# Kernel optimization log

Measured on AMD Instinct MI355X. Metric: run time of the kernel, lower is better.

## Reference

```python
import jax, jax.numpy as jnp
import numpy as np

B, N, E = 8, 2048, 2048  # requires N == E (see bmm(value, attn^T) constraint)

def setup_inputs() -> dict:
    key = jax.random.key(0)
    k1, k2, k3 = jax.random.split(key, 3)
    inputs = jax.random.normal(k1, (B, N, E), dtype=jnp.float32)
    # nn.Linear(embed_size, embed_size): weight [E,E], bias [E]
    W = jax.random.normal(k2, (E, E), dtype=jnp.float32) * (1.0 / np.sqrt(E))
    b = jax.random.normal(k3, (E,), dtype=jnp.float32) * 0.01
    gamma = jnp.zeros((), dtype=jnp.float32)  # nn.Parameter(torch.tensor(0.0))
    return {"inputs": inputs, "W": W, "b": b, "gamma": gamma}

def reference(inputs, W, b, gamma):
    # query = Linear(inputs); key = value = inputs
    query = jnp.einsum('bne,fe->bnf', inputs, W) + b          # [B,N,E]
    # scores = bmm(query, key^T) + gamma  -> [B,N,N]
    scores = jnp.einsum('bne,bme->bnm', query, inputs) + gamma
    # softmax over dim=1 (rows, NOT the usual last dim)
    attn = jax.nn.softmax(scores, axis=1)                      # [B,N,N]
    # output = bmm(value, attn^T): out[b,n,m] = sum_e value[b,n,e]*attn[b,m,e]
    out = jnp.einsum('bne,bme->bnm', inputs, attn)             # [B,N,N]
    return out
```

## Files before the change

kernel.cpp:

```cpp
#include <hip/hip_runtime.h>
#include <stdint.h>


typedef _Float16 f16;
typedef f16 f16x8 __attribute__((ext_vector_type(8)));
typedef f16 f16x4 __attribute__((ext_vector_type(4)));
typedef float f32x4 __attribute__((ext_vector_type(4)));

#define ND 2048
#define NNL 4194304L
#define NT 32

static __device__ __forceinline__ void stage16(const void* g, void* l) {
  __builtin_amdgcn_global_load_lds(
      (const __attribute__((address_space(1))) uint32_t*)g,
      (__attribute__((address_space(3))) uint32_t*)l, 16, 0, 0);
}

__global__ void cvt_f16(const float* __restrict__ x, f16* __restrict__ h, int n4) {
  int i = blockIdx.x * 256 + threadIdx.x;
  if (i >= n4) return;
  float4 v = reinterpret_cast<const float4*>(x)[i];
  f16x4 o;
  o.x = (f16)v.x; o.y = (f16)v.y; o.z = (f16)v.z; o.w = (f16)v.w;
  reinterpret_cast<f16x4*>(h)[i] = o;
}

#define RB(d_, o_, kh_) ((((d_) << 2) | ((o_) << 1) | (kh_)) * 16384)

#define STG(gp_, ro_, t_, kh_)                                           \
  do {                                                                   \
    stage16((gp_) + (long)(t_) * 128 + (kh_) * 64, smem + (ro_) + ld0);  \
    stage16((gp_) + 524288L + (long)(t_) * 128 + (kh_) * 64,             \
            smem + (ro_) + ld1);                                         \
  } while (0)

#define FENCE asm volatile("" ::: "memory")

#define SYNC(vm_)                                                        \
  do {                                                                   \
    asm volatile("s_waitcnt vmcnt(" #vm_ ") lgkmcnt(0)" ::: "memory");   \
    __builtin_amdgcn_s_barrier();                                        \
    FENCE;                                                               \
  } while (0)

#define PHASE(d_, mh_, kh_, RDB_, STAGE_)                                     \
  do {                                                                        \
    const char* ra_ = smem + RB(d_, 0, kh_) + (mh_) * 4096 + aoff;            \
    f16x8 af[4];                                                              \
    af[0] = *(const f16x8*)(ra_);                                             \
    af[1] = *(const f16x8*)(ra_ + 1024);                                      \
    af[2] = *(const f16x8*)(ra_ + 2048);                                      \
    af[3] = *(const f16x8*)(ra_ + 3072);                                      \
    if (RDB_) {                                                               \
      const char* rb_ = smem + RB(d_, 1, kh_) + boff;                         \
      bf[0] = *(const f16x8*)(rb_);                                           \
      bf[1] = *(const f16x8*)(rb_ + 1024);                                    \
      bf[2] = *(const f16x8*)(rb_ + 2048);                                    \
      bf[3] = *(const f16x8*)(rb_ + 3072);                                    \
    }                                                                         \
    STAGE_                                                                    \
    __builtin_amdgcn_s_setprio(1);                                            \
    _Pragma("unroll") for (int mt_ = 0; mt_ < 4; ++mt_) {                     \
      _Pragma("unroll") for (int nt_ = 0; nt_ < 4; ++nt_) {                   \
        acc[(mh_) * 4 + mt_][nt_] = __builtin_amdgcn_mfma_f32_16x16x32_f16(   \
            af[mt_], bf[nt_], acc[(mh_) * 4 + mt_][nt_], 0, 0, 0);            \
      }                                                                       \
    }                                                                         \
    __builtin_amdgcn_s_setprio(0);                                            \
  } while (0)

template <int MODE>
__launch_bounds__(512, 2) __global__
void gemm256(const f16* __restrict__ A, long sA, const f16* __restrict__ B, long sB,
             const float* __restrict__ bias, const float* __restrict__ gamma,
             float* __restrict__ Cf, f16* __restrict__ Ch,
             float* __restrict__ Mp, float* __restrict__ Sp) {
  __shared__ char smem[131072];

  const int bz = blockIdx.z;
  const int bx = ((blockIdx.x & 1) << 2) | (blockIdx.y & 3);
  const int by = (((blockIdx.x >> 1) & 3) << 1) | (blockIdx.y >> 2);
  const long tm = (long)by * 256;
  const long tn = (long)bx * 256;
  const int tid = threadIdx.x;
  const int lane = tid & 63;
  const int wid = tid >> 6;
  const int wm = (wid >> 2) << 7;
  const int wn = (wid & 3) << 6;

  const int sg = (tid & 3) ^ ((tid >> 3) & 3);
  const char* gA = (const char*)(A + bz * sA + tm * ND) + (long)(tid >> 2) * 4096 + sg * 16;
  const char* gB = (const char*)(B + bz * sB + tn * ND) + (long)(tid >> 2) * 4096 + sg * 16;
  const uint32_t ld0 = tid * 16u;
  const uint32_t ld1 = 8192u + tid * 16u;

  const int segsw = (((lane >> 4) ^ ((lane >> 1) & 3)) << 4);
  const int lrow = lane & 15;
  const int aoff = (wm + lrow) * 64 + segsw;
  const int boff = (wn + lrow) * 64 + segsw;

  f32x4 acc[8][4] = {};
  f16x8 bf[4];

  STG(gA, RB(0, 0, 0), 0, 0);
  STG(gB, RB(0, 1, 0), 0, 0);
  STG(gA, RB(0, 0, 1), 0, 1);
  STG(gB, RB(0, 1, 1), 0, 1);
  STG(gA, RB(1, 0, 0), 1, 0);
  STG(gB, RB(1, 1, 0), 1, 0);
  asm volatile("s_waitcnt vmcnt(8)" ::: "memory");
  __builtin_amdgcn_s_barrier();
  FENCE;

#pragma unroll 2
  for (int t = 0; t < NT - 2; ++t) {
    const int d = t & 1;
    const int e = d ^ 1;
    PHASE(d, 0, 0, 1, STG(gA, RB(e, 0, 1), t + 1, 1););
    PHASE(d, 1, 0, 0, STG(gB, RB(e, 1, 1), t + 1, 1););
    SYNC(8);
    PHASE(d, 0, 1, 1, STG(gA, RB(d, 0, 0), t + 2, 0););
    PHASE(d, 1, 1, 0, STG(gB, RB(d, 1, 0), t + 2, 0););
    SYNC(8);
  }
  {
    PHASE(0, 0, 0, 1, STG(gA, RB(1, 0, 1), NT - 1, 1););
    PHASE(0, 1, 0, 0, STG(gB, RB(1, 1, 1), NT - 1, 1););
    SYNC(8);
    PHASE(0, 0, 1, 1, ;);
    PHASE(0, 1, 1, 0, ;);
    SYNC(4);
  }
  {
    PHASE(1, 0, 0, 1, ;);
    PHASE(1, 1, 0, 0, ;);
    SYNC(0);
    PHASE(1, 0, 1, 1, ;);
    PHASE(1, 1, 1, 0, ;);
  }

  const int rr = (lane >> 4) << 2;
  const int cc = lane & 15;
  const long cb = (long)bz * NNL;
  if constexpr (MODE == 1) {
#pragma unroll
    for (int nt = 0; nt < 4; ++nt) {
      const long col = tn + wn + nt * 16 + cc;
      const float bj = bias[col];
#pragma unroll
      for (int mt = 0; mt < 8; ++mt) {
#pragma unroll
        for (int r = 0; r < 4; ++r) {
          const long row = tm + wm + mt * 16 + rr + r;
          Ch[cb + row * ND + col] = (f16)(acc[mt][nt][r] + bj);
        }
      }
    }
  } else if constexpr (MODE == 0) {
#pragma unroll
    for (int mt = 0; mt < 8; ++mt) {
#pragma unroll
      for (int nt = 0; nt < 4; ++nt) {
#pragma unroll
        for (int r = 0; r < 4; ++r) {
          const long row = tm + wm + mt * 16 + rr + r;
          const long col = tn + wn + nt * 16 + cc;
          Cf[cb + row * ND + col] = acc[mt][nt][r];
        }
      }
    }
  } else {
    const float g = gamma[0];
#pragma unroll
    for (int mt = 0; mt < 8; ++mt)
#pragma unroll
      for (int nt = 0; nt < 4; ++nt)
#pragma unroll
        for (int r = 0; r < 4; ++r)
          acc[mt][nt][r] = (float)(f16)(acc[mt][nt][r] + g);
    __syncthreads();
    float* redm = (float*)smem;
    float* reds = redm + 512;
#pragma unroll
    for (int nt = 0; nt < 4; ++nt) {
      float ml = -3.4e38f;
#pragma unroll
      for (int mt = 0; mt < 8; ++mt)
#pragma unroll
        for (int r = 0; r < 4; ++r)
          ml = fmaxf(ml, acc[mt][nt][r]);
      float sl = 0.f;
#pragma unroll
      for (int mt = 0; mt < 8; ++mt)
#pragma unroll
        for (int r = 0; r < 4; ++r)
          sl += __expf(acc[mt][nt][r] - ml);
#pragma unroll
      for (int off = 16; off < 64; off <<= 1) {
        float pm = __shfl_xor(ml, off, 64);
        float ps = __shfl_xor(sl, off, 64);
        float nm = fmaxf(ml, pm);
        sl = sl * __expf(ml - nm) + ps * __expf(pm - nm);
        ml = nm;
      }
      if ((lane >> 4) == 0) {
        redm[wid * 64 + nt * 16 + lrow] = ml;
        reds[wid * 64 + nt * 16 + lrow] = sl;
      }
    }
    __syncthreads();
    if (tid < 256) {
      const float mA = redm[tid], sA = reds[tid];
      const float mB = redm[256 + tid], sB = reds[256 + tid];
      const float m = fmaxf(mA, mB);
      const float s = sA * __expf(mA - m) + sB * __expf(mB - m);
      const long o = ((long)bz * 8 + by) * ND + tn + tid;
      Mp[o] = m;
      Sp[o] = s;
    }
#pragma unroll
    for (int mt = 0; mt < 8; ++mt) {
#pragma unroll
      for (int nt = 0; nt < 4; ++nt) {
#pragma unroll
        for (int r = 0; r < 4; ++r) {
          const long row = tm + wm + mt * 16 + rr + r;
          const long col = tn + wn + nt * 16 + cc;
          Ch[cb + row * ND + col] = (f16)acc[mt][nt][r];
        }
      }
    }
  }
}

__global__ void stats_combine(const float* __restrict__ Mp, const float* __restrict__ Sp,
                              float* __restrict__ Mx, float* __restrict__ Rs) {
  const int col = blockIdx.x * 256 + threadIdx.x;
  const int b = blockIdx.y;
  float m = -3.4e38f, s = 0.f;
  for (int k = 0; k < 8; ++k) {
    const long o = ((long)b * 8 + k) * ND + col;
    float mk = Mp[o], sk = Sp[o];
    float nm = fmaxf(m, mk);
    s = s * __expf(m - nm) + sk * __expf(mk - nm);
    m = nm;
  }
  Mx[(long)b * ND + col] = m;
  Rs[(long)b * ND + col] = 1.0f / s;
}

__global__ void scale_exp_kernel(const f16* __restrict__ S, const float* __restrict__ Mx,
                                 const float* __restrict__ Rs, f16* __restrict__ A) {
  const long i8 = (long)blockIdx.x * 256 + threadIdx.x;
  const long i = i8 * 8;
  const int b = (int)(i >> 22);
  const int col = (int)(i & 2047);
  f16x8 s = reinterpret_cast<const f16x8*>(S)[i8];
  const float* mp = &Mx[(long)b * ND + col];
  const float* rp = &Rs[(long)b * ND + col];
  float4 m0 = *reinterpret_cast<const float4*>(mp);
  float4 m1 = *reinterpret_cast<const float4*>(mp + 4);
  float4 r0 = *reinterpret_cast<const float4*>(rp);
  float4 r1 = *reinterpret_cast<const float4*>(rp + 4);
  f16x8 o;
  o[0] = (f16)(__expf((float)s[0] - m0.x) * r0.x);
  o[1] = (f16)(__expf((float)s[1] - m0.y) * r0.y);
  o[2] = (f16)(__expf((float)s[2] - m0.z) * r0.z);
  o[3] = (f16)(__expf((float)s[3] - m0.w) * r0.w);
  o[4] = (f16)(__expf((float)s[4] - m1.x) * r1.x);
  o[5] = (f16)(__expf((float)s[5] - m1.y) * r1.y);
  o[6] = (f16)(__expf((float)s[6] - m1.z) * r1.z);
  o[7] = (f16)(__expf((float)s[7] - m1.w) * r1.w);
  reinterpret_cast<f16x8*>(A)[i8] = o;
}

extern "C" void kernel_launch(void* const* d_in, const int* in_sizes, int n_in,
                              void* d_out, int out_size, void* d_ws, size_t ws_size,
                              hipStream_t stream) {
  (void)in_sizes; (void)n_in; (void)out_size;
  const float* X = (const float*)d_in[0];
  const float* W = (const float*)d_in[1];
  const float* bias = (const float*)d_in[2];
  const float* gamma = (const float*)d_in[3];

  char* ws = (char*)d_ws;
  f16* Xh = (f16*)(ws);
  f16* Wh = (f16*)(ws + 67108864L);
  f16* Qh = (f16*)(ws + 75497472L);
  f16* Sh = (f16*)(ws + 142606336L);
  float* Mp = (float*)(ws + 276824064L);
  float* Sp = (float*)(ws + 277348352L);
  float* Mx = (float*)(ws + 277872640L);
  float* Rs = (float*)(ws + 277938176L);
  f16* Amat = Qh;
  if (ws_size < 278003712UL) return;

  cvt_f16<<<32768, 256, 0, stream>>>(X, Xh, 8388608);
  cvt_f16<<<4096, 256, 0, stream>>>(W, Wh, 1048576);

  dim3 gg(8, 8, 8), bb(512);
  gemm256<1><<<gg, bb, 0, stream>>>(Xh, NNL, Wh, 0L, bias, nullptr, nullptr, Qh,
                                    nullptr, nullptr);
  gemm256<2><<<gg, bb, 0, stream>>>(Qh, NNL, Xh, NNL, nullptr, gamma, nullptr, Sh,
                                    Mp, Sp);
  stats_combine<<<dim3(8, 8), 256, 0, stream>>>(Mp, Sp, Mx, Rs);
  scale_exp_kernel<<<16384, 256, 0, stream>>>(Sh, Mx, Rs, Amat);
  gemm256<0><<<gg, bb, 0, stream>>>(Xh, NNL, Amat, NNL, nullptr, nullptr,
                                    (float*)d_out, nullptr, nullptr, nullptr);
}
```

Baseline: 627.6 us.

## Software-pipeline LDS fragment reads ahead of MFMAs and use grid-stride conversion

The GEMM main loop now reads the next A/B fragments from LDS into extra register sets before issuing the current MFMA block. This hides LDS read latency behind matrix math and lets the barrier waits use a smaller vmcnt threshold. The conversion kernels become grid-stride loops with fewer blocks. The extra fragment registers raise register pressure under the 512x2 launch bounds, and the looser vmcnt waits assume the staging order stays correct.

Result: no change. 634.2 us (+1.0%).

```diff
diff --git a/kernel.cpp b/kernel.cpp
--- a/kernel.cpp
+++ b/kernel.cpp
@@ -17,13 +17,14 @@
       (__attribute__((address_space(3))) uint32_t*)l, 16, 0, 0);
 }
 
-__global__ void cvt_f16(const float* __restrict__ x, f16* __restrict__ h, int n4) {
-  int i = blockIdx.x * 256 + threadIdx.x;
-  if (i >= n4) return;
-  float4 v = reinterpret_cast<const float4*>(x)[i];
-  f16x4 o;
-  o.x = (f16)v.x; o.y = (f16)v.y; o.z = (f16)v.z; o.w = (f16)v.w;
-  reinterpret_cast<f16x4*>(h)[i] = o;
+__global__ void cvt_f16(const float* __restrict__ x, f16* __restrict__ h, long n4) {
+  const long stride = (long)gridDim.x * 256;
+  for (long i = (long)blockIdx.x * 256 + threadIdx.x; i < n4; i += stride) {
+    float4 v = reinterpret_cast<const float4*>(x)[i];
+    f16x4 o;
+    o.x = (f16)v.x; o.y = (f16)v.y; o.z = (f16)v.z; o.w = (f16)v.w;
+    reinterpret_cast<f16x4*>(h)[i] = o;
+  }
 }
 
 #define RB(d_, o_, kh_) ((((d_) << 2) | ((o_) << 1) | (kh_)) * 16384)
@@ -44,31 +45,37 @@
     FENCE;                                                               \
   } while (0)
 
-#define PHASE(d_, mh_, kh_, RDB_, STAGE_)                                     \
+#define RDA(dst_, d_, kh_, mh_)                                          \
+  do {                                                                   \
+    const char* p_ = smem + RB(d_, 0, kh_) + (mh_) * 4096 + aoff;        \
+    (dst_).v[0] = *(const f16x8*)(p_);                                   \
+    (dst_).v[1] = *(const f16x8*)(p_ + 1024);                            \
+    (dst_).v[2] = *(const f16x8*)(p_ + 2048);                            \
+    (dst_).v[3] = *(const f16x8*)(p_ + 3072);                            \
+  } while (0)
+
+#define RDBF(dst_, d_, kh_)                                              \
+  do {                                                                   \
+    const char* p_ = smem + RB(d_, 1, kh_) + boff;                       \
+    (dst_).v[0] = *(const f16x8*)(p_);                                   \
+    (dst_).v[1] = *(const f16x8*)(p_ + 1024);                            \
+    (dst_).v[2] = *(const f16x8*)(p_ + 2048);                            \
+    (dst_).v[3] = *(const f16x8*)(p_ + 3072);                            \
+  } while (0)
+
+#define MM(mh_, A_, B_)                                                       \
   do {                                                                        \
-    const char* ra_ = smem + RB(d_, 0, kh_) + (mh_) * 4096 + aoff;            \
-    f16x8 af[4];                                                              \
-    af[0] = *(const f16x8*)(ra_);                                             \
-    af[1] = *(const f16x8*)(ra_ + 1024);                                      \
-    af[2] = *(const f16x8*)(ra_ + 2048);                                      \
-    af[3] = *(const f16x8*)(ra_ + 3072);                                      \
-    if (RDB_) {                                                               \
-      const char* rb_ = smem + RB(d_, 1, kh_) + boff;                         \
-      bf[0] = *(const f16x8*)(rb_);                                           \
-      bf[1] = *(const f16x8*)(rb_ + 1024);                                    \
-      bf[2] = *(const f16x8*)(rb_ + 2048);                                    \
-      bf[3] = *(const f16x8*)(rb_ + 3072);                                    \
-    }                                                                         \
-    STAGE_                                                                    \
     __builtin_amdgcn_s_setprio(1);                                            \
     _Pragma("unroll") for (int mt_ = 0; mt_ < 4; ++mt_) {                     \
       _Pragma("unroll") for (int nt_ = 0; nt_ < 4; ++nt_) {                   \
         acc[(mh_) * 4 + mt_][nt_] = __builtin_amdgcn_mfma_f32_16x16x32_f16(   \
-            af[mt_], bf[nt_], acc[(mh_) * 4 + mt_][nt_], 0, 0, 0);            \
+            (A_).v[mt_], (B_).v[nt_], acc[(mh_) * 4 + mt_][nt_], 0, 0, 0);    \
       }                                                                       \
     }                                                                         \
     __builtin_amdgcn_s_setprio(0);                                            \
   } while (0)
+
+struct frag4 { f16x8 v[4]; };
 
 template <int MODE>
 __launch_bounds__(512, 2) __global__
@@ -101,7 +108,7 @@
   const int boff = (wn + lrow) * 64 + segsw;
 
   f32x4 acc[8][4] = {};
-  f16x8 bf[4];
+  frag4 aX, aY, aZ, bX, bY;
 
   STG(gA, RB(0, 0, 0), 0, 0);
   STG(gB, RB(0, 1, 0), 0, 0);
@@ -109,35 +116,59 @@
   STG(gB, RB(0, 1, 1), 0, 1);
   STG(gA, RB(1, 0, 0), 1, 0);
   STG(gB, RB(1, 1, 0), 1, 0);
-  asm volatile("s_waitcnt vmcnt(8)" ::: "memory");
+  asm volatile("s_waitcnt vmcnt(4)" ::: "memory");
   __builtin_amdgcn_s_barrier();
   FENCE;
+  RDA(aX, 0, 0, 0);
+  RDBF(bX, 0, 0);
 
 #pragma unroll 2
   for (int t = 0; t < NT - 2; ++t) {
     const int d = t & 1;
     const int e = d ^ 1;
-    PHASE(d, 0, 0, 1, STG(gA, RB(e, 0, 1), t + 1, 1););
-    PHASE(d, 1, 0, 0, STG(gB, RB(e, 1, 1), t + 1, 1););
-    SYNC(8);
-    PHASE(d, 0, 1, 1, STG(gA, RB(d, 0, 0), t + 2, 0););
-    PHASE(d, 1, 1, 0, STG(gB, RB(d, 1, 0), t + 2, 0););
-    SYNC(8);
+    RDA(aY, d, 0, 1);
+    STG(gA, RB(e, 0, 1), t + 1, 1);
+    MM(0, aX, bX);
+    RDA(aZ, d, 1, 0);
+    RDBF(bY, d, 1);
+    STG(gB, RB(e, 1, 1), t + 1, 1);
+    MM(1, aY, bX);
+    SYNC(4);
+    RDA(aY, d, 1, 1);
+    STG(gA, RB(d, 0, 0), t + 2, 0);
+    MM(0, aZ, bY);
+    RDA(aX, e, 0, 0);
+    RDBF(bX, e, 0);
+    STG(gB, RB(d, 1, 0), t + 2, 0);
+    MM(1, aY, bY);
+    SYNC(4);
   }
   {
-    PHASE(0, 0, 0, 1, STG(gA, RB(1, 0, 1), NT - 1, 1););
-    PHASE(0, 1, 0, 0, STG(gB, RB(1, 1, 1), NT - 1, 1););
-    SYNC(8);
-    PHASE(0, 0, 1, 1, ;);
-    PHASE(0, 1, 1, 0, ;);
+    RDA(aY, 0, 0, 1);
+    STG(gA, RB(1, 0, 1), NT - 1, 1);
+    MM(0, aX, bX);
+    RDA(aZ, 0, 1, 0);
+    RDBF(bY, 0, 1);
+    STG(gB, RB(1, 1, 1), NT - 1, 1);
+    MM(1, aY, bX);
     SYNC(4);
+    RDA(aY, 0, 1, 1);
+    MM(0, aZ, bY);
+    RDA(aX, 1, 0, 0);
+    RDBF(bX, 1, 0);
+    MM(1, aY, bY);
+    SYNC(0);
   }
   {
-    PHASE(1, 0, 0, 1, ;);
-    PHASE(1, 1, 0, 0, ;);
+    RDA(aY, 1, 0, 1);
+    MM(0, aX, bX);
+    RDA(aZ, 1, 1, 0);
+    RDBF(bY, 1, 1);
+    MM(1, aY, bX);
     SYNC(0);
-    PHASE(1, 0, 1, 1, ;);
-    PHASE(1, 1, 1, 0, ;);
+    RDA(aY, 1, 1, 1);
+    MM(0, aZ, bY);
+    MM(1, aY, bY);
   }
 
   const int rr = (lane >> 4) << 2;
@@ -296,8 +327,8 @@
   f16* Amat = Qh;
   if (ws_size < 278003712UL) return;
 
-  cvt_f16<<<32768, 256, 0, stream>>>(X, Xh, 8388608);
-  cvt_f16<<<4096, 256, 0, stream>>>(W, Wh, 1048576);
+  cvt_f16<<<2048, 256, 0, stream>>>(X, Xh, 8388608L);
+  cvt_f16<<<2048, 256, 0, stream>>>(W, Wh, 1048576L);
 
   dim3 gg(8, 8, 8), bb(512);
   gemm256<1><<<gg, bb, 0, stream>>>(Xh, NNL, Wh, 0L, bias, nullptr, nullptr, Qh,
```

## Use 1024-thread blocks with 16 waves each computing 64x64 subtiles

Applied to the files above, without the earlier changes.

The 256x256 GEMM tile moves from 8 waves (each 128x64 with two M-half phases) to 16 waves of 64x64 each. Every thread now issues one staging load per operand per k-half, and the wait counts and the cross-wave softmax reduction are changed to match. The aim is more waves to hide latency and lower per-thread register pressure. In exchange, each wave re-reads B fragments from LDS, total LDS read traffic per tile goes up, and occupancy drops to one block per CU given the 128KB of shared memory.

After: 625.4 us. No clear change (-0.4%).

```diff
diff --git a/kernel.cpp b/kernel.cpp
--- a/kernel.cpp
+++ b/kernel.cpp
@@ -28,12 +28,8 @@
 
 #define RB(d_, o_, kh_) ((((d_) << 2) | ((o_) << 1) | (kh_)) * 16384)
 
-#define STG(gp_, ro_, t_, kh_)                                           \
-  do {                                                                   \
-    stage16((gp_) + (long)(t_) * 128 + (kh_) * 64, smem + (ro_) + ld0);  \
-    stage16((gp_) + 524288L + (long)(t_) * 128 + (kh_) * 64,             \
-            smem + (ro_) + ld1);                                         \
-  } while (0)
+#define STG(gp_, ro_, t_, kh_) \
+  stage16((gp_) + (long)(t_) * 128 + (kh_) * 64, smem + (ro_) + ld0)
 
 #define FENCE asm volatile("" ::: "memory")
 
@@ -44,34 +40,28 @@
     FENCE;                                                               \
   } while (0)
 
-#define PHASE(d_, mh_, kh_, RDB_, STAGE_)                                     \
+#define PHASE(d_, kh_, STAGE_)                                                \
   do {                                                                        \
-    const char* ra_ = smem + RB(d_, 0, kh_) + (mh_) * 4096 + aoff;            \
-    f16x8 af[4];                                                              \
-    af[0] = *(const f16x8*)(ra_);                                             \
-    af[1] = *(const f16x8*)(ra_ + 1024);                                      \
-    af[2] = *(const f16x8*)(ra_ + 2048);                                      \
-    af[3] = *(const f16x8*)(ra_ + 3072);                                      \
-    if (RDB_) {                                                               \
-      const char* rb_ = smem + RB(d_, 1, kh_) + boff;                         \
-      bf[0] = *(const f16x8*)(rb_);                                           \
-      bf[1] = *(const f16x8*)(rb_ + 1024);                                    \
-      bf[2] = *(const f16x8*)(rb_ + 2048);                                    \
-      bf[3] = *(const f16x8*)(rb_ + 3072);                                    \
+    const char* ra_ = smem + RB(d_, 0, kh_) + aoff;                           \
+    const char* rb_ = smem + RB(d_, 1, kh_) + boff;                           \
+    f16x8 af[4], bf[4];                                                       \
+    _Pragma("unroll") for (int i_ = 0; i_ < 4; ++i_) {                        \
+      af[i_] = *(const f16x8*)(ra_ + i_ * 1024);                              \
+      bf[i_] = *(const f16x8*)(rb_ + i_ * 1024);                              \
     }                                                                         \
     STAGE_                                                                    \
     __builtin_amdgcn_s_setprio(1);                                            \
     _Pragma("unroll") for (int mt_ = 0; mt_ < 4; ++mt_) {                     \
       _Pragma("unroll") for (int nt_ = 0; nt_ < 4; ++nt_) {                   \
-        acc[(mh_) * 4 + mt_][nt_] = __builtin_amdgcn_mfma_f32_16x16x32_f16(   \
-            af[mt_], bf[nt_], acc[(mh_) * 4 + mt_][nt_], 0, 0, 0);            \
+        acc[mt_][nt_] = __builtin_amdgcn_mfma_f32_16x16x32_f16(               \
+            af[mt_], bf[nt_], acc[mt_][nt_], 0, 0, 0);                        \
       }                                                                       \
     }                                                                         \
     __builtin_amdgcn_s_setprio(0);                                            \
   } while (0)
 
 template <int MODE>
-__launch_bounds__(512, 2) __global__
+__launch_bounds__(1024) __global__
 void gemm256(const f16* __restrict__ A, long sA, const f16* __restrict__ B, long sB,
              const float* __restrict__ bias, const float* __restrict__ gamma,
              float* __restrict__ Cf, f16* __restrict__ Ch,
@@ -86,22 +76,20 @@
   const int tid = threadIdx.x;
   const int lane = tid & 63;
   const int wid = tid >> 6;
-  const int wm = (wid >> 2) << 7;
+  const int wm = (wid >> 2) << 6;
   const int wn = (wid & 3) << 6;
 
   const int sg = (tid & 3) ^ ((tid >> 3) & 3);
   const char* gA = (const char*)(A + bz * sA + tm * ND) + (long)(tid >> 2) * 4096 + sg * 16;
   const char* gB = (const char*)(B + bz * sB + tn * ND) + (long)(tid >> 2) * 4096 + sg * 16;
   const uint32_t ld0 = tid * 16u;
-  const uint32_t ld1 = 8192u + tid * 16u;
 
   const int segsw = (((lane >> 4) ^ ((lane >> 1) & 3)) << 4);
   const int lrow = lane & 15;
   const int aoff = (wm + lrow) * 64 + segsw;
   const int boff = (wn + lrow) * 64 + segsw;
 
-  f32x4 acc[8][4] = {};
-  f16x8 bf[4];
+  f32x4 acc[4][4] = {};
 
   STG(gA, RB(0, 0, 0), 0, 0);
   STG(gB, RB(0, 1, 0), 0, 0);
@@ -109,7 +97,7 @@
   STG(gB, RB(0, 1, 1), 0, 1);
   STG(gA, RB(1, 0, 0), 1, 0);
   STG(gB, RB(1, 1, 0), 1, 0);
-  asm volatile("s_waitcnt vmcnt(8)" ::: "memory");
+  asm volatile("s_waitcnt vmcnt(4)" ::: "memory");
   __builtin_amdgcn_s_barrier();
   FENCE;
 
@@ -117,27 +105,21 @@
   for (int t = 0; t < NT - 2; ++t) {
     const int d = t & 1;
     const int e = d ^ 1;
-    PHASE(d, 0, 0, 1, STG(gA, RB(e, 0, 1), t + 1, 1););
-    PHASE(d, 1, 0, 0, STG(gB, RB(e, 1, 1), t + 1, 1););
-    SYNC(8);
-    PHASE(d, 0, 1, 1, STG(gA, RB(d, 0, 0), t + 2, 0););
-    PHASE(d, 1, 1, 0, STG(gB, RB(d, 1, 0), t + 2, 0););
-    SYNC(8);
+    PHASE(d, 0, STG(gA, RB(e, 0, 1), t + 1, 1); STG(gB, RB(e, 1, 1), t + 1, 1););
+    SYNC(4);
+    PHASE(d, 1, STG(gA, RB(d, 0, 0), t + 2, 0); STG(gB, RB(d, 1, 0), t + 2, 0););
+    SYNC(4);
   }
   {
-    PHASE(0, 0, 0, 1, STG(gA, RB(1, 0, 1), NT - 1, 1););
-    PHASE(0, 1, 0, 0, STG(gB, RB(1, 1, 1), NT - 1, 1););
-    SYNC(8);
-    PHASE(0, 0, 1, 1, ;);
-    PHASE(0, 1, 1, 0, ;);
+    PHASE(0, 0, STG(gA, RB(1, 0, 1), NT - 1, 1); STG(gB, RB(1, 1, 1), NT - 1, 1););
     SYNC(4);
+    PHASE(0, 1, ;);
+    SYNC(2);
   }
   {
-    PHASE(1, 0, 0, 1, ;);
-    PHASE(1, 1, 0, 0, ;);
+    PHASE(1, 0, ;);
     SYNC(0);
-    PHASE(1, 0, 1, 1, ;);
-    PHASE(1, 1, 1, 0, ;);
+    PHASE(1, 1, ;);
   }
 
   const int rr = (lane >> 4) << 2;
@@ -149,7 +131,7 @@
       const long col = tn + wn + nt * 16 + cc;
       const float bj = bias[col];
 #pragma unroll
-      for (int mt = 0; mt < 8; ++mt) {
+      for (int mt = 0; mt < 4; ++mt) {
 #pragma unroll
         for (int r = 0; r < 4; ++r) {
           const long row = tm + wm + mt * 16 + rr + r;
@@ -159,7 +141,7 @@
     }
   } else if constexpr (MODE == 0) {
 #pragma unroll
-    for (int mt = 0; mt < 8; ++mt) {
+    for (int mt = 0; mt < 4; ++mt) {
 #pragma unroll
       for (int nt = 0; nt < 4; ++nt) {
 #pragma unroll
@@ -173,7 +155,7 @@
   } else {
     const float g = gamma[0];
 #pragma unroll
-    for (int mt = 0; mt < 8; ++mt)
+    for (int mt = 0; mt < 4; ++mt)
 #pragma unroll
       for (int nt = 0; nt < 4; ++nt)
 #pragma unroll
@@ -181,18 +163,18 @@
           acc[mt][nt][r] = (float)(f16)(acc[mt][nt][r] + g);
     __syncthreads();
     float* redm = (float*)smem;
-    float* reds = redm + 512;
+    float* reds = redm + 1024;
 #pragma unroll
     for (int nt = 0; nt < 4; ++nt) {
       float ml = -3.4e38f;
 #pragma unroll
-      for (int mt = 0; mt < 8; ++mt)
+      for (int mt = 0; mt < 4; ++mt)
 #pragma unroll
         for (int r = 0; r < 4; ++r)
           ml = fmaxf(ml, acc[mt][nt][r]);
       float sl = 0.f;
 #pragma unroll
-      for (int mt = 0; mt < 8; ++mt)
+      for (int mt = 0; mt < 4; ++mt)
 #pragma unroll
         for (int r = 0; r < 4; ++r)
           sl += __expf(acc[mt][nt][r] - ml);
@@ -211,16 +193,25 @@
     }
     __syncthreads();
     if (tid < 256) {
-      const float mA = redm[tid], sA = reds[tid];
-      const float mB = redm[256 + tid], sB = reds[256 + tid];
-      const float m = fmaxf(mA, mB);
-      const float s = sA * __expf(mA - m) + sB * __expf(mB - m);
+      const int wbase = (tid >> 6);
+      const int ntc = (tid >> 4) & 3;
+      const int ccc = tid & 15;
+      float m = -3.4e38f, s = 0.f;
+#pragma unroll
+      for (int k = 0; k < 4; ++k) {
+        const int w = wbase + 4 * k;
+        const float mk = redm[w * 64 + ntc * 16 + ccc];
+        const float sk = reds[w * 64 + ntc * 16 + ccc];
+        const float nm = fmaxf(m, mk);
+        s = s * __expf(m - nm) + sk * __expf(mk - nm);
+        m = nm;
+      }
       const long o = ((long)bz * 8 + by) * ND + tn + tid;
       Mp[o] = m;
       Sp[o] = s;
     }
 #pragma unroll
-    for (int mt = 0; mt < 8; ++mt) {
+    for (int mt = 0; mt < 4; ++mt) {
 #pragma unroll
       for (int nt = 0; nt < 4; ++nt) {
 #pragma unroll
@@ -299,7 +290,7 @@
   cvt_f16<<<32768, 256, 0, stream>>>(X, Xh, 8388608);
   cvt_f16<<<4096, 256, 0, stream>>>(W, Wh, 1048576);
 
-  dim3 gg(8, 8, 8), bb(512);
+  dim3 gg(8, 8, 8), bb(1024);
   gemm256<1><<<gg, bb, 0, stream>>>(Xh, NNL, Wh, 0L, bias, nullptr, nullptr, Qh,
                                     nullptr, nullptr);
   gemm256<2><<<gg, bb, 0, stream>>>(Qh, NNL, Xh, NNL, nullptr, gamma, nullptr, Sh,
```
